# Kernel optimization log

Hardware: AMD Instinct MI355X
Metric: run time of the kernel (lower is better)

Reference implementation:

```python
import jax, jax.numpy as jnp
import numpy as np

EMBED = 1024
HEADS = 16
HEAD_SIZE = EMBED // HEADS
B, T = 2, 2048
EPS = 1e-5


def layer_norm(x, g, b):
    mu = jnp.mean(x, axis=-1, keepdims=True)
    var = jnp.var(x, axis=-1, keepdims=True)
    return (x - mu) * jax.lax.rsqrt(var + EPS) * g + b


def setup_inputs() -> dict:
    key = jax.random.key(0)
    ks = jax.random.split(key, 12)
    s = 0.02
    return {
        "x": jax.random.normal(ks[0], (B, T, EMBED), jnp.float32),
        "Wq": s * jax.random.normal(ks[1], (EMBED, EMBED), jnp.float32),
        "Wk": s * jax.random.normal(ks[2], (EMBED, EMBED), jnp.float32),
        "Wv": s * jax.random.normal(ks[3], (EMBED, EMBED), jnp.float32),
        "Wo": s * jax.random.normal(ks[4], (EMBED, EMBED), jnp.float32),
        "bo": jnp.zeros((EMBED,), jnp.float32),
        "W1": s * jax.random.normal(ks[5], (EMBED, 4 * EMBED), jnp.float32),
        "b1": jnp.zeros((4 * EMBED,), jnp.float32),
        "W2": s * jax.random.normal(ks[6], (4 * EMBED, EMBED), jnp.float32),
        "b2": jnp.zeros((EMBED,), jnp.float32),
        "ln1_g": jnp.ones((EMBED,), jnp.float32),
        "ln1_b": jnp.zeros((EMBED,), jnp.float32),
        "ln2_g": jnp.ones((EMBED,), jnp.float32),
        "ln2_b": jnp.zeros((EMBED,), jnp.float32),
    }


def reference(x, Wq, Wk, Wv, Wo, bo, W1, b1, W2, b2, ln1_g, ln1_b, ln2_g, ln2_b):
    # --- multi-head causal self-attention on ln1(x) ---
    h = layer_norm(x, ln1_g, ln1_b)                      # [B,T,D]
    q = (h @ Wq).reshape(B, T, HEADS, HEAD_SIZE)         # per-head Q (concat layout)
    k = (h @ Wk).reshape(B, T, HEADS, HEAD_SIZE)
    v = (h @ Wv).reshape(B, T, HEADS, HEAD_SIZE)
    scores = jnp.einsum("bqhd,bkhd->bhqk", q, k) / jnp.sqrt(
        jnp.asarray(HEAD_SIZE, x.dtype)
    )                                                    # [B,H,T,T]
    causal = jnp.tril(jnp.ones((T, T), bool))
    scores = jnp.where(causal, scores, -jnp.inf)
    wei = jax.nn.softmax(scores, axis=-1)
    attn = jnp.einsum("bhqk,bkhd->bqhd", wei, v).reshape(B, T, EMBED)
    x = x + attn @ Wo + bo                               # residual (dropout=0)
    # --- feed-forward on ln2(x) ---
    h2 = layer_norm(x, ln2_g, ln2_b)
    ff = jax.nn.relu(h2 @ W1 + b1) @ W2 + b2
    return x + ff
```

## Files before the change

kernel.cpp:

```cpp
#include <hip/hip_runtime.h>


typedef __bf16 bf16;
typedef __attribute__((ext_vector_type(8))) __bf16 bf16x8;
typedef __attribute__((ext_vector_type(4))) __bf16 bf16x4;
typedef __attribute__((ext_vector_type(4))) short  shortx4;
typedef __attribute__((ext_vector_type(4))) float  floatx4;

__device__ __forceinline__ short f2bf_bits(float x) {
  return __builtin_bit_cast(short, (bf16)x);
}

__device__ __forceinline__ void gl2lds16(const bf16* g, bf16* l) {
  __builtin_amdgcn_global_load_lds((const __attribute__((address_space(1))) void*)g,
                                   (__attribute__((address_space(3))) void*)l, 16, 0, 0);
}

__device__ __forceinline__ void barx() {
  asm volatile("" ::: "memory");
  __builtin_amdgcn_s_barrier();
  asm volatile("" ::: "memory");
}

__global__ __launch_bounds__(256) void prep_kernel(
    const float* __restrict__ Wq, const float* __restrict__ Wk,
    const float* __restrict__ Wv, const float* __restrict__ Wo,
    const float* __restrict__ W1, const float* __restrict__ W2,
    bf16* __restrict__ WqkvT, bf16* __restrict__ WoT,
    bf16* __restrict__ W1T, bf16* __restrict__ W2T,
    const float* __restrict__ x, const float* __restrict__ ln1g,
    const float* __restrict__ ln1b, bf16* __restrict__ h1)
{
  int id = blockIdx.x;
  if (id >= 12288) {
    const int row = id - 12288, t = threadIdx.x;
    const float* xr = x + (size_t)row * 1024;
    float4 v = *(const float4*)(xr + t * 4);
    float s  = v.x + v.y + v.z + v.w;
    float s2 = v.x * v.x + v.y * v.y + v.z * v.z + v.w * v.w;
    #pragma unroll
    for (int off = 1; off < 64; off <<= 1) {
      s  += __shfl_xor(s, off);
      s2 += __shfl_xor(s2, off);
    }
    __shared__ float ps[4], ps2[4];
    int wv = t >> 6;
    if ((t & 63) == 0) { ps[wv] = s; ps2[wv] = s2; }
    __syncthreads();
    s  = ps[0] + ps[1] + ps[2] + ps[3];
    s2 = ps2[0] + ps2[1] + ps2[2] + ps2[3];
    const float mu = s * (1.0f / 1024.0f);
    const float rstd = rsqrtf(s2 * (1.0f / 1024.0f) - mu * mu + 1e-5f);
    float4 gv = *(const float4*)(ln1g + t * 4);
    float4 bv = *(const float4*)(ln1b + t * 4);
    bf16x4 o;
    o[0] = (bf16)((v.x - mu) * rstd * gv.x + bv.x);
    o[1] = (bf16)((v.y - mu) * rstd * gv.y + bv.y);
    o[2] = (bf16)((v.z - mu) * rstd * gv.z + bv.z);
    o[3] = (bf16)((v.w - mu) * rstd * gv.w + bv.w);
    *(bf16x4*)(h1 + (size_t)row * 1024 + t * 4) = o;
    return;
  }
  const float* src; bf16* dst; int K, N, tile;
  if (id < 4096) {
    K = 1024; N = 1024; tile = id & 1023;
    int wsel = id >> 10;
    src = (wsel == 0) ? Wq : (wsel == 1) ? Wk : (wsel == 2) ? Wv : Wo;
    dst = (wsel < 3) ? (WqkvT + (size_t)wsel * 1024 * 1024) : WoT;
  } else if (id < 8192) {
    K = 1024; N = 4096; tile = id - 4096; src = W1; dst = W1T;
  } else {
    K = 4096; N = 1024; tile = id - 8192; src = W2; dst = W2T;
  }
  int ntn = N >> 5;
  int k0 = (tile / ntn) * 32, n0 = (tile % ntn) * 32;
  __shared__ float tl[32][33];
  int tr = threadIdx.x >> 3, tc = (threadIdx.x & 7) * 4;
  float4 v = *(const float4*)(src + (size_t)(k0 + tr) * N + n0 + tc);
  tl[tr][tc + 0] = v.x; tl[tr][tc + 1] = v.y; tl[tr][tc + 2] = v.z; tl[tr][tc + 3] = v.w;
  __syncthreads();
  bf16x4 o = { (bf16)tl[tc + 0][tr], (bf16)tl[tc + 1][tr],
               (bf16)tl[tc + 2][tr], (bf16)tl[tc + 3][tr] };
  *(bf16x4*)(dst + (size_t)(n0 + tr) * K + k0 + tc) = o;
}

__device__ __forceinline__ void gemm_core(
    const bf16* __restrict__ A, const bf16* __restrict__ Bt,
    int Ktot, int k0, int k1, bf16* As, bf16* Bs, floatx4 (&acc)[4][4])
{
  const int tid = threadIdx.x, lane = tid & 63, wv = tid >> 6;
  const int li = lane & 15, g = lane >> 4;
  const int wm = wv >> 1, wn = wv & 1;
  const int srow = wv * 16 + (lane >> 2);
  const int scol = (lane & 3) * 8;
  const bf16* aP = A  + (size_t)srow * Ktot + scol;
  const bf16* bP = Bt + (size_t)srow * Ktot + scol;
  bf16* AsW = As + wv * 512;
  bf16* BsW = Bs + wv * 512;
  for (int kt = k0; kt < k1; kt += 64) {
    gl2lds16(aP + kt,                          AsW);
    gl2lds16(aP + kt + (size_t)64 * Ktot,      AsW + 2048);
    gl2lds16(aP + kt + 32,                     AsW + 4096);
    gl2lds16(aP + kt + 32 + (size_t)64 * Ktot, AsW + 6144);
    gl2lds16(bP + kt,                          BsW);
    gl2lds16(bP + kt + (size_t)64 * Ktot,      BsW + 2048);
    gl2lds16(bP + kt + 32,                     BsW + 4096);
    gl2lds16(bP + kt + 32 + (size_t)64 * Ktot, BsW + 6144);
    __syncthreads();
    #pragma unroll
    for (int hh = 0; hh < 2; ++hh) {
      const bf16* Ap = As + hh * 4096;
      const bf16* Bp = Bs + hh * 4096;
      bf16x8 af[4], bfr[4];
      #pragma unroll
      for (int r = 0; r < 4; ++r)
        af[r] = *(const bf16x8*)(Ap + (wm * 64 + r * 16 + li) * 32 + g * 8);
      #pragma unroll
      for (int c = 0; c < 4; ++c)
        bfr[c] = *(const bf16x8*)(Bp + (wn * 64 + c * 16 + li) * 32 + g * 8);
      #pragma unroll
      for (int r = 0; r < 4; ++r)
        #pragma unroll
        for (int c = 0; c < 4; ++c)
          acc[r][c] = __builtin_amdgcn_mfma_f32_16x16x32_bf16(bfr[c], af[r], acc[r][c], 0, 0, 0);
    }
    __syncthreads();
  }
}

__global__ __launch_bounds__(256) void gemm_splitk(
    const bf16* __restrict__ A, const bf16* __restrict__ Bt,
    bf16* __restrict__ Cp, int M, int N, int Ktot, int Kc)
{
  __shared__ bf16 As[8192];
  __shared__ bf16 Bs[8192];
  const int lane = threadIdx.x & 63, wv = threadIdx.x >> 6;
  const int li = lane & 15, g = lane >> 4;
  const int m0 = blockIdx.x * 128, n0 = blockIdx.y * 128;
  const int z = blockIdx.z;
  const int wm = wv >> 1, wn = wv & 1;
  floatx4 acc[4][4] = {};
  gemm_core(A + (size_t)m0 * Ktot, Bt + (size_t)n0 * Ktot, Ktot,
            z * Kc, (z + 1) * Kc, As, Bs, acc);
  bf16* C = Cp + (size_t)z * M * N;
  #pragma unroll
  for (int r = 0; r < 4; ++r) {
    int rowC = m0 + wm * 64 + r * 16 + li;
    #pragma unroll
    for (int c = 0; c < 4; ++c) {
      int colC = n0 + wn * 64 + c * 16 + g * 4;
      bf16x4 ov = { (bf16)acc[r][c][0], (bf16)acc[r][c][1],
                    (bf16)acc[r][c][2], (bf16)acc[r][c][3] };
      *(bf16x4*)(C + (size_t)rowC * N + colC) = ov;
    }
  }
}

#define MFMA_PHASE(RH, CH, BB)                                                  \
  do {                                                                          \
    __builtin_amdgcn_s_setprio(1);                                              \
    _Pragma("unroll") for (int ks = 0; ks < 2; ++ks)                            \
      _Pragma("unroll") for (int r = 0; r < 4; ++r)                             \
        _Pragma("unroll") for (int c = 0; c < 2; ++c)                           \
          acc[(RH) * 4 + r][(CH) * 2 + c] =                                     \
            __builtin_amdgcn_mfma_f32_16x16x32_bf16(                            \
                BB[c][ks], af[r][ks], acc[(RH) * 4 + r][(CH) * 2 + c], 0, 0, 0);\
    __builtin_amdgcn_s_setprio(0);                                              \
  } while (0)

__device__ __forceinline__ void gemm8_core(
    const bf16* __restrict__ A, const bf16* __restrict__ Bt,
    int K, int k0, int k1, bf16* lds, floatx4 (&acc)[8][4])
{
  const int lane = threadIdx.x & 63, wv = threadIdx.x >> 6;
  const int li = lane & 15, g = lane >> 4;
  const int wm2 = wv >> 2, wn4 = wv & 3;
  const int nt = (k1 - k0) >> 6;

  const int srow  = wv * 16 + (lane >> 3);
  const int schnk = ((lane & 7) ^ (lane >> 3)) * 8;
  const bf16* aSrc = A  + (size_t)srow * K + k0 + schnk;
  const bf16* bSrc = Bt + (size_t)srow * K + k0 + schnk;
  const size_t row8 = (size_t)8 * K;
  bf16* ldsB = lds + 32768;

  const int xk0 = ((0 + g) ^ (li & 7)) * 8;
  const int xk1 = ((4 + g) ^ (li & 7)) * 8;

  auto stA = [&](int t, int h) {
    if (t < nt) {
      const bf16* gp = aSrc + (size_t)(h * 128) * K + (t << 6);
      bf16* lp = lds + (((t & 1) * 2 + h) << 13) + wv * 1024;
      gl2lds16(gp, lp);
      gl2lds16(gp + row8, lp + 512);
    }
  };
  auto stB = [&](int t, int h) {
    if (t < nt) {
      const bf16* gp = bSrc + (size_t)(h * 128) * K + (t << 6);
      bf16* lp = ldsB + (((t & 1) * 2 + h) << 13) + wv * 1024;
      gl2lds16(gp, lp);
      gl2lds16(gp + row8, lp + 512);
    }
  };

  bf16x8 af[4][2], bA[2][2], bB[2][2];
  auto ldA = [&](int b, int RH) {
    const bf16* base = lds + ((b * 2 + RH) << 13) + (wm2 * 64 + li) * 64;
    #pragma unroll
    for (int r = 0; r < 4; ++r) {
      af[r][0] = *(const bf16x8*)(base + r * 1024 + xk0);
      af[r][1] = *(const bf16x8*)(base + r * 1024 + xk1);
    }
  };
  auto ldB = [&](int b, int CH, bf16x8 (&bb)[2][2]) {
    const bf16* base = ldsB + ((b * 2 + CH) << 13) + (wn4 * 32 + li) * 64;
    #pragma unroll
    for (int c = 0; c < 2; ++c) {
      bb[c][0] = *(const bf16x8*)(base + c * 1024 + xk0);
      bb[c][1] = *(const bf16x8*)(base + c * 1024 + xk1);
    }
  };

  stA(0, 0); stB(0, 0); stB(0, 1); stA(0, 1);
  stA(1, 0); stB(1, 0);
  asm volatile("s_waitcnt vmcnt(4)" ::: "memory");
  barx();

  for (int t = 0; t < nt; ++t) {
    const int b = t & 1;
    ldA(b, 0); ldB(b, 0, bA);
    stB(t + 1, 1);
    barx();
    MFMA_PHASE(0, 0, bA);
    barx();
    ldB(b, 1, bB);
    stA(t + 1, 1);
    asm volatile("s_waitcnt vmcnt(8)" ::: "memory");
    barx();
    MFMA_PHASE(0, 1, bB);
    barx();
    ldA(b, 1);
    stA(t + 2, 0);
    barx();
    MFMA_PHASE(1, 0, bA);
    barx();
    stB(t + 2, 0);
    asm volatile("s_waitcnt vmcnt(6)" ::: "memory");
    barx();
    MFMA_PHASE(1, 1, bB);
    barx();
  }
}

__global__ __launch_bounds__(512, 2) void gemm8_ffn1(
    const bf16* __restrict__ A, const bf16* __restrict__ Bt,
    const float* __restrict__ bias, bf16* __restrict__ C,
    int M, int N, int K)
{
  __shared__ bf16 lds8[65536];
  const int m0 = blockIdx.x * 256, n0 = blockIdx.y * 256;
  floatx4 acc[8][4] = {};
  gemm8_core(A + (size_t)m0 * K, Bt + (size_t)n0 * K, K, 0, K, lds8, acc);
  const int lane = threadIdx.x & 63, wv = threadIdx.x >> 6;
  const int li = lane & 15, g = lane >> 4;
  const int wm2 = wv >> 2, wn4 = wv & 3;
  #pragma unroll
  for (int ar = 0; ar < 8; ++ar) {
    int rowC = m0 + (ar >> 2) * 128 + wm2 * 64 + (ar & 3) * 16 + li;
    #pragma unroll
    for (int ac = 0; ac < 4; ++ac) {
      int colC = n0 + (ac >> 1) * 128 + wn4 * 32 + (ac & 1) * 16 + g * 4;
      float4 bv = *(const float4*)(bias + colC);
      bf16x4 ov = { (bf16)fmaxf(acc[ar][ac][0] + bv.x, 0.f),
                    (bf16)fmaxf(acc[ar][ac][1] + bv.y, 0.f),
                    (bf16)fmaxf(acc[ar][ac][2] + bv.z, 0.f),
                    (bf16)fmaxf(acc[ar][ac][3] + bv.w, 0.f) };
      *(bf16x4*)(C + (size_t)rowC * N + colC) = ov;
    }
  }
}

__global__ __launch_bounds__(512, 2) void gemm8_qkv(
    const bf16* __restrict__ A, const bf16* __restrict__ Bt,
    bf16* __restrict__ qkv, bf16* __restrict__ VtG)
{
  const int K = 1024;
  __shared__ bf16 lds8[65536];
  const int m0 = blockIdx.x * 256, n0 = blockIdx.y * 256;
  floatx4 acc[8][4] = {};
  gemm8_core(A + (size_t)m0 * K, Bt + (size_t)n0 * K, K, 0, K, lds8, acc);
  const int lane = threadIdx.x & 63, wv = threadIdx.x >> 6;
  const int li = lane & 15, g = lane >> 4;
  const int wm2 = wv >> 2, wn4 = wv & 3;
  if (n0 < 2048) {
    #pragma unroll
    for (int ar = 0; ar < 8; ++ar) {
      int rowC = m0 + (ar >> 2) * 128 + wm2 * 64 + (ar & 3) * 16 + li;
      #pragma unroll
      for (int ac = 0; ac < 4; ++ac) {
        int colC = n0 + (ac >> 1) * 128 + wn4 * 32 + (ac & 1) * 16 + g * 4;
        bf16x4 ov = { (bf16)acc[ar][ac][0], (bf16)acc[ar][ac][1],
                      (bf16)acc[ar][ac][2], (bf16)acc[ar][ac][3] };
        *(bf16x4*)(qkv + (size_t)rowC * 3072 + colC) = ov;
      }
    }
  } else {
    #pragma unroll
    for (int ar = 0; ar < 8; ++ar) {
      int rowC = m0 + (ar >> 2) * 128 + wm2 * 64 + (ar & 3) * 16 + li;
      int key = rowC & 2047, bq = rowC >> 11;
      #pragma unroll
      for (int ac = 0; ac < 4; ++ac) {
        int vcol0 = n0 + (ac >> 1) * 128 + wn4 * 32 + (ac & 1) * 16 + g * 4 - 2048;
        #pragma unroll
        for (int e = 0; e < 4; ++e) {
          int vcol = vcol0 + e;
          int hh = vcol >> 6, d = vcol & 63;
          VtG[((size_t)(bq * 16 + hh) * 64 + d) * 2048 + key] = (bf16)acc[ar][ac][e];
        }
      }
    }
  }
}

__global__ __launch_bounds__(512, 2) void gemm8_splitk(
    const bf16* __restrict__ A, const bf16* __restrict__ Bt,
    bf16* __restrict__ Cp, int M, int N, int Ktot, int Kc)
{
  __shared__ bf16 lds8[65536];
  const int m0 = blockIdx.x * 256, n0 = blockIdx.y * 256;
  const int z = blockIdx.z;
  floatx4 acc[8][4] = {};
  gemm8_core(A + (size_t)m0 * Ktot, Bt + (size_t)n0 * Ktot, Ktot,
             z * Kc, (z + 1) * Kc, lds8, acc);
  const int lane = threadIdx.x & 63, wv = threadIdx.x >> 6;
  const int li = lane & 15, g = lane >> 4;
  const int wm2 = wv >> 2, wn4 = wv & 3;
  bf16* C = Cp + (size_t)z * M * N;
  #pragma unroll
  for (int ar = 0; ar < 8; ++ar) {
    int rowC = m0 + (ar >> 2) * 128 + wm2 * 64 + (ar & 3) * 16 + li;
    #pragma unroll
    for (int ac = 0; ac < 4; ++ac) {
      int colC = n0 + (ac >> 1) * 128 + wn4 * 32 + (ac & 1) * 16 + g * 4;
      bf16x4 ov = { (bf16)acc[ar][ac][0], (bf16)acc[ar][ac][1],
                    (bf16)acc[ar][ac][2], (bf16)acc[ar][ac][3] };
      *(bf16x4*)(C + (size_t)rowC * N + colC) = ov;
    }
  }
}

__global__ __launch_bounds__(256) void combine_wo_ln2(
    const bf16* __restrict__ P, const float* __restrict__ bo,
    const float* __restrict__ x, const float* __restrict__ gam,
    const float* __restrict__ bet, float* __restrict__ x2, bf16* __restrict__ h2)
{
  const int row = blockIdx.x, t = threadIdx.x;
  const size_t base = (size_t)row * 1024 + t * 4;
  float4 v = *(const float4*)(x + base);
  bf16x4 p0 = *(const bf16x4*)(P + base);
  bf16x4 p1 = *(const bf16x4*)(P + 4194304 + base);
  float4 bv = *(const float4*)(bo + t * 4);
  v.x += (float)p0[0] + (float)p1[0] + bv.x;
  v.y += (float)p0[1] + (float)p1[1] + bv.y;
  v.z += (float)p0[2] + (float)p1[2] + bv.z;
  v.w += (float)p0[3] + (float)p1[3] + bv.w;
  *(float4*)(x2 + base) = v;
  float s  = v.x + v.y + v.z + v.w;
  float s2 = v.x * v.x + v.y * v.y + v.z * v.z + v.w * v.w;
  #pragma unroll
  for (int off = 1; off < 64; off <<= 1) {
    s  += __shfl_xor(s, off);
    s2 += __shfl_xor(s2, off);
  }
  __shared__ float ps[4], ps2[4];
  int wv = t >> 6;
  if ((t & 63) == 0) { ps[wv] = s; ps2[wv] = s2; }
  __syncthreads();
  s  = ps[0] + ps[1] + ps[2] + ps[3];
  s2 = ps2[0] + ps2[1] + ps2[2] + ps2[3];
  const float mu = s * (1.0f / 1024.0f);
  const float rstd = rsqrtf(s2 * (1.0f / 1024.0f) - mu * mu + 1e-5f);
  float4 gv = *(const float4*)(gam + t * 4);
  float4 bb = *(const float4*)(bet + t * 4);
  bf16x4 o;
  o[0] = (bf16)((v.x - mu) * rstd * gv.x + bb.x);
  o[1] = (bf16)((v.y - mu) * rstd * gv.y + bb.y);
  o[2] = (bf16)((v.z - mu) * rstd * gv.z + bb.z);
  o[3] = (bf16)((v.w - mu) * rstd * gv.w + bb.w);
  *(bf16x4*)(h2 + base) = o;
}

__global__ __launch_bounds__(256) void combine_ffn2(
    const bf16* __restrict__ P, const float* __restrict__ b2,
    const float* __restrict__ x2, float* __restrict__ out)
{
  const size_t i = ((size_t)blockIdx.x * 256 + threadIdx.x) * 4;
  const int col = (int)(i & 1023);
  float4 acc = *(const float4*)(x2 + i);
  float4 bv = *(const float4*)(b2 + col);
  acc.x += bv.x; acc.y += bv.y; acc.z += bv.z; acc.w += bv.w;
  #pragma unroll
  for (int z = 0; z < 4; ++z) {
    bf16x4 p = *(const bf16x4*)(P + (size_t)z * 4194304 + i);
    acc.x += (float)p[0]; acc.y += (float)p[1];
    acc.z += (float)p[2]; acc.w += (float)p[3];
  }
  *(float4*)(out + i) = acc;
}

__global__ __launch_bounds__(256, 2) void attn_kernel(
    const bf16* __restrict__ qkv, const bf16* __restrict__ VtG,
    bf16* __restrict__ attnb)
{
  __shared__ bf16 Ks[2][128 * 72];
  __shared__ bf16 Vt[2][64 * 136];
  const int t = threadIdx.x, lane = t & 63, wv = t >> 6;
  const int li = lane & 15, g = lane >> 4;
  const int xl = blockIdx.x & 7;
  const int r_ = blockIdx.x >> 3;
  const int g2 = r_ & 3, p = r_ >> 2;
  const int bh = g2 * 8 + xl;
  const int b = bh >> 4, h = bh & 15;
  const int row0 = b << 11;
  const int tlo = p * 4 + wv, thi = 127 - tlo;
  const int q0l = tlo << 4, q0h = thi << 4;
  const size_t qkvbase = (size_t)row0 * 3072 + (size_t)h * 64;
  const bf16* vgbase = VtG + (size_t)(b * 16 + h) * 64 * 2048;

  const bf16* qpl = qkv + qkvbase + (size_t)(q0l + li) * 3072 + g * 8;
  const bf16* qph = qkv + qkvbase + (size_t)(q0h + li) * 3072 + g * 8;
  bf16x8 bl0 = *(const bf16x8*)(qpl), bl1 = *(const bf16x8*)(qpl + 32);
  bf16x8 bh0 = *(const bf16x8*)(qph), bh1 = *(const bf16x8*)(qph + 32);

  floatx4 ol[4] = {}, oh[4] = {};
  float ll = 0.f, lh = 0.f;
  const int cmax = 31 - p;
  const int CC = (cmax + 2) >> 1;

  const int krow0 = t >> 3, kdc = (t & 7) * 8;
  const int vd = t >> 2, vkg = (t & 3) * 16;
  bf16x8 kv0, kv1, kv2, kv3, vv0, vv1, vv2, vv3;

  auto ld = [&](int cc) {
    const size_t kb = qkvbase + (size_t)(cc * 128) * 3072 + 1024;
    kv0 = *(const bf16x8*)(qkv + kb + (size_t)(krow0     ) * 3072 + kdc);
    kv1 = *(const bf16x8*)(qkv + kb + (size_t)(krow0 + 32) * 3072 + kdc);
    kv2 = *(const bf16x8*)(qkv + kb + (size_t)(krow0 + 64) * 3072 + kdc);
    kv3 = *(const bf16x8*)(qkv + kb + (size_t)(krow0 + 96) * 3072 + kdc);
    const bf16* vg = vgbase + (size_t)vd * 2048 + cc * 128 + vkg;
    vv0 = *(const bf16x8*)(vg);
    vv1 = *(const bf16x8*)(vg + 8);
    vv2 = *(const bf16x8*)(vg + 64);
    vv3 = *(const bf16x8*)(vg + 72);
  };
  auto wr = [&](int buf) {
    *(bf16x8*)(Ks[buf] + (krow0     ) * 72 + kdc) = kv0;
    *(bf16x8*)(Ks[buf] + (krow0 + 32) * 72 + kdc) = kv1;
    *(bf16x8*)(Ks[buf] + (krow0 + 64) * 72 + kdc) = kv2;
    *(bf16x8*)(Ks[buf] + (krow0 + 96) * 72 + kdc) = kv3;
    *(bf16x8*)(Vt[buf] + vd * 136 + vkg)      = vv0;
    *(bf16x8*)(Vt[buf] + vd * 136 + vkg + 8)  = vv1;
    *(bf16x8*)(Vt[buf] + vd * 136 + vkg + 64) = vv2;
    *(bf16x8*)(Vt[buf] + vd * 136 + vkg + 72) = vv3;
  };

  auto proc = [&](const bf16* KsB, const bf16* VtB, int h64,
                  const bf16x8& bq0, const bf16x8& bq1, float& l_i,
                  floatx4 (&o)[4], int qg, int k0, bool diag) {
    floatx4 sv[4];
    #pragma unroll
    for (int s = 0; s < 4; ++s) {
      const bf16* kr = KsB + (h64 * 64 + s * 16 + li) * 72 + g * 8;
      bf16x8 a0 = *(const bf16x8*)(kr);
      bf16x8 a1 = *(const bf16x8*)(kr + 32);
      floatx4 z = {0.f, 0.f, 0.f, 0.f};
      z = __builtin_amdgcn_mfma_f32_16x16x32_bf16(a0, bq0, z, 0, 0, 0);
      z = __builtin_amdgcn_mfma_f32_16x16x32_bf16(a1, bq1, z, 0, 0, 0);
      sv[s] = z;
    }
    float pv[4][4];
    float rs = 0.f;
    #pragma unroll
    for (int s = 0; s < 4; ++s)
      #pragma unroll
      for (int e = 0; e < 4; ++e) {
        float val = __expf(sv[s][e] * 0.125f - 4.0f);
        if (diag) {
          int kg = k0 + s * 16 + g * 4 + e;
          val = (kg <= qg) ? val : 0.0f;
        }
        pv[s][e] = val;
        rs += val;
      }
    rs += __shfl_xor(rs, 16);
    rs += __shfl_xor(rs, 32);
    l_i += rs;
    #pragma unroll
    for (int s = 0; s < 4; ++s) {
      shortx4 bp = { f2bf_bits(pv[s][0]), f2bf_bits(pv[s][1]),
                     f2bf_bits(pv[s][2]), f2bf_bits(pv[s][3]) };
      #pragma unroll
      for (int c = 0; c < 4; ++c) {
        shortx4 av = *(const shortx4*)(VtB + (c * 16 + li) * 136 + h64 * 64 + s * 16 + g * 4);
        o[c] = __builtin_amdgcn_mfma_f32_16x16x16bf16_1k(av, bp, o[c], 0, 0, 0);
      }
    }
  };

  ld(0);
  wr(0);
  __syncthreads();
  int buf = 0;
  for (int cc = 0; cc < CC; ++cc) {
    if (cc + 1 < CC) ld(cc + 1);
    const int c0 = cc * 2, c1 = c0 + 1;
    proc(Ks[buf], Vt[buf], 0, bh0, bh1, lh, oh, q0h + li, c0 * 64, c0 == cmax);
    if (c0 <= p) proc(Ks[buf], Vt[buf], 0, bl0, bl1, ll, ol, q0l + li, c0 * 64, c0 == p);
    if (c1 <= cmax) {
      proc(Ks[buf], Vt[buf], 1, bh0, bh1, lh, oh, q0h + li, c1 * 64, c1 == cmax);
      if (c1 <= p) proc(Ks[buf], Vt[buf], 1, bl0, bl1, ll, ol, q0l + li, c1 * 64, c1 == p);
    }
    if (cc + 1 < CC) wr(buf ^ 1);
    __syncthreads();
    buf ^= 1;
  }

  const float invh = 1.0f / lh, invl = 1.0f / ll;
  #pragma unroll
  for (int c = 0; c < 4; ++c) {
    bf16x4 ovh = { (bf16)(oh[c][0] * invh), (bf16)(oh[c][1] * invh),
                   (bf16)(oh[c][2] * invh), (bf16)(oh[c][3] * invh) };
    *(bf16x4*)(attnb + (size_t)(row0 + q0h + li) * 1024 + h * 64 + c * 16 + g * 4) = ovh;
    bf16x4 ovl = { (bf16)(ol[c][0] * invl), (bf16)(ol[c][1] * invl),
                   (bf16)(ol[c][2] * invl), (bf16)(ol[c][3] * invl) };
    *(bf16x4*)(attnb + (size_t)(row0 + q0l + li) * 1024 + h * 64 + c * 16 + g * 4) = ovl;
  }
}

extern "C" void kernel_launch(void* const* d_in, const int* in_sizes, int n_in,
                              void* d_out, int out_size, void* d_ws, size_t ws_size,
                              hipStream_t stream) {
  (void)in_sizes; (void)n_in; (void)out_size; (void)ws_size;
  const float* x    = (const float*)d_in[0];
  const float* Wq   = (const float*)d_in[1];
  const float* Wk   = (const float*)d_in[2];
  const float* Wv   = (const float*)d_in[3];
  const float* Wo   = (const float*)d_in[4];
  const float* bo   = (const float*)d_in[5];
  const float* W1   = (const float*)d_in[6];
  const float* b1   = (const float*)d_in[7];
  const float* W2   = (const float*)d_in[8];
  const float* b2   = (const float*)d_in[9];
  const float* ln1g = (const float*)d_in[10];
  const float* ln1b = (const float*)d_in[11];
  const float* ln2g = (const float*)d_in[12];
  const float* ln2b = (const float*)d_in[13];
  float* out = (float*)d_out;
  char* ws = (char*)d_ws;

  constexpr size_t OFF_WQKVT = 0;
  constexpr size_t OFF_WOT   = OFF_WQKVT + 3072ull * 1024 * 2;
  constexpr size_t OFF_W1T   = OFF_WOT   + 1024ull * 1024 * 2;
  constexpr size_t OFF_W2T   = OFF_W1T   + 4096ull * 1024 * 2;
  constexpr size_t OFF_H1    = OFF_W2T   + 1024ull * 4096 * 2;
  constexpr size_t OFF_QKV   = OFF_H1    + 4096ull * 1024 * 2;
  constexpr size_t OFF_ATT   = OFF_QKV   + 4096ull * 3072 * 2;
  constexpr size_t OFF_X2    = OFF_ATT   + 4096ull * 1024 * 2;
  constexpr size_t OFF_H2    = OFF_X2    + 4096ull * 1024 * 4;
  constexpr size_t OFF_F1    = OFF_H2    + 4096ull * 1024 * 2;
  constexpr size_t OFF_PART  = OFF_F1    + 4096ull * 4096 * 2;
  constexpr size_t OFF_VTG   = OFF_PART  + 4ull * 4096 * 1024 * 2;

  bf16*  WqkvT = (bf16*)(ws + OFF_WQKVT);
  bf16*  WoT   = (bf16*)(ws + OFF_WOT);
  bf16*  W1T   = (bf16*)(ws + OFF_W1T);
  bf16*  W2T   = (bf16*)(ws + OFF_W2T);
  bf16*  h1    = (bf16*)(ws + OFF_H1);
  bf16*  qkv   = (bf16*)(ws + OFF_QKV);
  bf16*  attnb = (bf16*)(ws + OFF_ATT);
  float* x2    = (float*)(ws + OFF_X2);
  bf16*  h2    = (bf16*)(ws + OFF_H2);
  bf16*  f1    = (bf16*)(ws + OFF_F1);
  bf16*  part  = (bf16*)(ws + OFF_PART);
  bf16*  vtg   = (bf16*)(ws + OFF_VTG);

  prep_kernel<<<16384, 256, 0, stream>>>(Wq, Wk, Wv, Wo, W1, W2,
                                         WqkvT, WoT, W1T, W2T, x, ln1g, ln1b, h1);
  gemm8_qkv<<<dim3(16, 12), 512, 0, stream>>>(h1, WqkvT, qkv, vtg);
  attn_kernel<<<512, 256, 0, stream>>>(qkv, vtg, attnb);
  gemm_splitk<<<dim3(32, 8, 2), 256, 0, stream>>>(attnb, WoT, part, 4096, 1024, 1024, 512);
  combine_wo_ln2<<<4096, 256, 0, stream>>>(part, bo, x, ln2g, ln2b, x2, h2);
  gemm8_ffn1<<<dim3(16, 16), 512, 0, stream>>>(h2, W1T, b1, f1, 4096, 4096, 1024);
  gemm8_splitk<<<dim3(16, 4, 4), 512, 0, stream>>>(f1, W2T, part, 4096, 1024, 4096, 1024);
  combine_ffn2<<<4096, 256, 0, stream>>>(part, b2, x2, out);
}
```

Baseline: 317.7 us.

## Fuse high/low query tiles in attention and add XCD-aware GEMM block swizzle

The attention inner loop now processes the paired high and low query tiles together when both are active for a key chunk. Each K and V fragment is read from LDS once and feeds MFMAs for both tiles, which halves LDS reads and interleaves independent MFMA chains. Separately, the three GEMM kernels remap linear block IDs so that consecutive blocks scheduled on the same XCD cover neighbouring tiles, aiming for better L2 reuse. The fused path raises register pressure, which could hurt occupancy at 2 blocks per CU.

```diff
diff --git a/kernel.cpp b/kernel.cpp
--- a/kernel.cpp
+++ b/kernel.cpp
@@ -253,13 +253,21 @@
   }
 }
 
+__device__ __forceinline__ void xcd_swz(int lin, int nwg, int nbx, int& bx, int& by) {
+  int lin2 = (lin & 7) * (nwg >> 3) + (lin >> 3);
+  bx = lin2 % nbx;
+  by = lin2 / nbx;
+}
+
 __global__ __launch_bounds__(512, 2) void gemm8_ffn1(
     const bf16* __restrict__ A, const bf16* __restrict__ Bt,
     const float* __restrict__ bias, bf16* __restrict__ C,
     int M, int N, int K)
 {
   __shared__ bf16 lds8[65536];
-  const int m0 = blockIdx.x * 256, n0 = blockIdx.y * 256;
+  int bx, by;
+  xcd_swz(blockIdx.y * gridDim.x + blockIdx.x, gridDim.x * gridDim.y, gridDim.x, bx, by);
+  const int m0 = bx * 256, n0 = by * 256;
   floatx4 acc[8][4] = {};
   gemm8_core(A + (size_t)m0 * K, Bt + (size_t)n0 * K, K, 0, K, lds8, acc);
   const int lane = threadIdx.x & 63, wv = threadIdx.x >> 6;
@@ -287,7 +295,9 @@
 {
   const int K = 1024;
   __shared__ bf16 lds8[65536];
-  const int m0 = blockIdx.x * 256, n0 = blockIdx.y * 256;
+  int bx, by;
+  xcd_swz(blockIdx.y * gridDim.x + blockIdx.x, gridDim.x * gridDim.y, gridDim.x, bx, by);
+  const int m0 = bx * 256, n0 = by * 256;
   floatx4 acc[8][4] = {};
   gemm8_core(A + (size_t)m0 * K, Bt + (size_t)n0 * K, K, 0, K, lds8, acc);
   const int lane = threadIdx.x & 63, wv = threadIdx.x >> 6;
@@ -329,7 +339,9 @@
     bf16* __restrict__ Cp, int M, int N, int Ktot, int Kc)
 {
   __shared__ bf16 lds8[65536];
-  const int m0 = blockIdx.x * 256, n0 = blockIdx.y * 256;
+  int bx, by;
+  xcd_swz(blockIdx.y * gridDim.x + blockIdx.x, gridDim.x * gridDim.y, gridDim.x, bx, by);
+  const int m0 = bx * 256, n0 = by * 256;
   const int z = blockIdx.z;
   floatx4 acc[8][4] = {};
   gemm8_core(A + (size_t)m0 * Ktot, Bt + (size_t)n0 * Ktot, Ktot,
@@ -466,9 +478,7 @@
     *(bf16x8*)(Vt[buf] + vd * 136 + vkg + 72) = vv3;
   };
 
-  auto proc = [&](const bf16* KsB, const bf16* VtB, int h64,
-                  const bf16x8& bq0, const bf16x8& bq1, float& l_i,
-                  floatx4 (&o)[4], int qg, int k0, bool diag) {
+  auto proc1 = [&](const bf16* KsB, const bf16* VtB, int h64, int k0, bool diag) {
     floatx4 sv[4];
     #pragma unroll
     for (int s = 0; s < 4; ++s) {
@@ -476,12 +486,13 @@
       bf16x8 a0 = *(const bf16x8*)(kr);
       bf16x8 a1 = *(const bf16x8*)(kr + 32);
       floatx4 z = {0.f, 0.f, 0.f, 0.f};
-      z = __builtin_amdgcn_mfma_f32_16x16x32_bf16(a0, bq0, z, 0, 0, 0);
-      z = __builtin_amdgcn_mfma_f32_16x16x32_bf16(a1, bq1, z, 0, 0, 0);
+      z = __builtin_amdgcn_mfma_f32_16x16x32_bf16(a0, bh0, z, 0, 0, 0);
+      z = __builtin_amdgcn_mfma_f32_16x16x32_bf16(a1, bh1, z, 0, 0, 0);
       sv[s] = z;
     }
     float pv[4][4];
     float rs = 0.f;
+    const int qg = q0h + li;
     #pragma unroll
     for (int s = 0; s < 4; ++s)
       #pragma unroll
@@ -496,7 +507,7 @@
       }
     rs += __shfl_xor(rs, 16);
     rs += __shfl_xor(rs, 32);
-    l_i += rs;
+    lh += rs;
     #pragma unroll
     for (int s = 0; s < 4; ++s) {
       shortx4 bp = { f2bf_bits(pv[s][0]), f2bf_bits(pv[s][1]),
@@ -504,7 +515,62 @@
       #pragma unroll
       for (int c = 0; c < 4; ++c) {
         shortx4 av = *(const shortx4*)(VtB + (c * 16 + li) * 136 + h64 * 64 + s * 16 + g * 4);
-        o[c] = __builtin_amdgcn_mfma_f32_16x16x16bf16_1k(av, bp, o[c], 0, 0, 0);
+        oh[c] = __builtin_amdgcn_mfma_f32_16x16x16bf16_1k(av, bp, oh[c], 0, 0, 0);
+      }
+    }
+  };
+
+  auto proc2 = [&](const bf16* KsB, const bf16* VtB, int h64, int k0, bool diagL) {
+    floatx4 svh[4], svl[4];
+    #pragma unroll
+    for (int s = 0; s < 4; ++s) {
+      const bf16* kr = KsB + (h64 * 64 + s * 16 + li) * 72 + g * 8;
+      bf16x8 a0 = *(const bf16x8*)(kr);
+      bf16x8 a1 = *(const bf16x8*)(kr + 32);
+      floatx4 zh = {0.f, 0.f, 0.f, 0.f};
+      zh = __builtin_amdgcn_mfma_f32_16x16x32_bf16(a0, bh0, zh, 0, 0, 0);
+      zh = __builtin_amdgcn_mfma_f32_16x16x32_bf16(a1, bh1, zh, 0, 0, 0);
+      svh[s] = zh;
+      floatx4 zl = {0.f, 0.f, 0.f, 0.f};
+      zl = __builtin_amdgcn_mfma_f32_16x16x32_bf16(a0, bl0, zl, 0, 0, 0);
+      zl = __builtin_amdgcn_mfma_f32_16x16x32_bf16(a1, bl1, zl, 0, 0, 0);
+      svl[s] = zl;
+    }
+    float pvh[4][4], pvl[4][4];
+    float rsh = 0.f, rsl = 0.f;
+    const int qgl = q0l + li;
+    #pragma unroll
+    for (int s = 0; s < 4; ++s)
+      #pragma unroll
+      for (int e = 0; e < 4; ++e) {
+        float vh = __expf(svh[s][e] * 0.125f - 4.0f);
+        pvh[s][e] = vh;
+        rsh += vh;
+        float vl = __expf(svl[s][e] * 0.125f - 4.0f);
+        if (diagL) {
+          int kg = k0 + s * 16 + g * 4 + e;
+          vl = (kg <= qgl) ? vl : 0.0f;
+        }
+        pvl[s][e] = vl;
+        rsl += vl;
+      }
+    rsh += __shfl_xor(rsh, 16);
+    rsh += __shfl_xor(rsh, 32);
+    lh += rsh;
+    rsl += __shfl_xor(rsl, 16);
+    rsl += __shfl_xor(rsl, 32);
+    ll += rsl;
+    #pragma unroll
+    for (int s = 0; s < 4; ++s) {
+      shortx4 bph = { f2bf_bits(pvh[s][0]), f2bf_bits(pvh[s][1]),
+                      f2bf_bits(pvh[s][2]), f2bf_bits(pvh[s][3]) };
+      shortx4 bpl = { f2bf_bits(pvl[s][0]), f2bf_bits(pvl[s][1]),
+                      f2bf_bits(pvl[s][2]), f2bf_bits(pvl[s][3]) };
+      #pragma unroll
+      for (int c = 0; c < 4; ++c) {
+        shortx4 av = *(const shortx4*)(VtB + (c * 16 + li) * 136 + h64 * 64 + s * 16 + g * 4);
+        oh[c] = __builtin_amdgcn_mfma_f32_16x16x16bf16_1k(av, bph, oh[c], 0, 0, 0);
+        ol[c] = __builtin_amdgcn_mfma_f32_16x16x16bf16_1k(av, bpl, ol[c], 0, 0, 0);
       }
     }
   };
@@ -516,11 +582,11 @@
   for (int cc = 0; cc < CC; ++cc) {
     if (cc + 1 < CC) ld(cc + 1);
     const int c0 = cc * 2, c1 = c0 + 1;
-    proc(Ks[buf], Vt[buf], 0, bh0, bh1, lh, oh, q0h + li, c0 * 64, c0 == cmax);
-    if (c0 <= p) proc(Ks[buf], Vt[buf], 0, bl0, bl1, ll, ol, q0l + li, c0 * 64, c0 == p);
+    if (c0 <= p) proc2(Ks[buf], Vt[buf], 0, c0 * 64, c0 == p);
+    else         proc1(Ks[buf], Vt[buf], 0, c0 * 64, c0 == cmax);
     if (c1 <= cmax) {
-      proc(Ks[buf], Vt[buf], 1, bh0, bh1, lh, oh, q0h + li, c1 * 64, c1 == cmax);
-      if (c1 <= p) proc(Ks[buf], Vt[buf], 1, bl0, bl1, ll, ol, q0l + li, c1 * 64, c1 == p);
+      if (c1 <= p) proc2(Ks[buf], Vt[buf], 1, c1 * 64, c1 == p);
+      else         proc1(Ks[buf], Vt[buf], 1, c1 * 64, c1 == cmax);
     }
     if (cc + 1 < CC) wr(buf ^ 1);
     __syncthreads();
```

Result: no change. 319.2 us (+0.5%).
